# Kernel tuning notes

Measured on AMD Instinct MI355X. Metric: run time of the kernel, lower is better.

Reference implementation:

```python
import jax, jax.numpy as jnp
import numpy as np

H, NOPE, ROPE, VD, KV_LORA, HID = 16, 128, 64, 128, 512, 2048
QK = NOPE + ROPE
SCALE = QK ** -0.5
EPS = 1e-5


def _rope(x, freqs):
    # x: [b, t, h, ROPE]; freqs: [t, ROPE//2] angles. Complex-pair rotation.
    cos = jnp.cos(freqs)[None, :, None, :]
    sin = jnp.sin(freqs)[None, :, None, :]
    xr = x.reshape(x.shape[:-1] + (ROPE // 2, 2))
    x1, x2 = xr[..., 0], xr[..., 1]
    o1 = x1 * cos - x2 * sin
    o2 = x1 * sin + x2 * cos
    return jnp.stack([o1, o2], axis=-1).reshape(x.shape)


def _layernorm(x, g, b):
    mu = jnp.mean(x, axis=-1, keepdims=True)
    var = jnp.var(x, axis=-1, keepdims=True)
    return (x - mu) * jax.lax.rsqrt(var + EPS) * g + b


def setup_inputs() -> dict:
    key = jax.random.key(0)
    ks = jax.random.split(key, 6)
    b, t = 2, 2048

    def xavier(k, shape):
        fan_in, fan_out = shape
        lim = np.sqrt(6.0 / (fan_in + fan_out))
        return jax.random.uniform(k, shape, jnp.float32, -lim, lim)

    hidden_states = jax.random.normal(ks[0], (b, t, HID), jnp.float32)
    # rope angles: theta_i = 10000^(-2i/ROPE), angle[p,i] = p * theta_i
    inv_freq = 1.0 / (10000.0 ** (np.arange(0, ROPE, 2, dtype=np.float32) / ROPE))
    freqs = jnp.asarray(np.arange(t, dtype=np.float32)[:, None] * inv_freq[None, :])
    # causal additive mask broadcastable to [b,t,s,h]
    causal = jnp.where(jnp.arange(t)[None, :] <= jnp.arange(t)[:, None], 0.0, -1e9)
    attention_mask = causal.astype(jnp.float32)[None, :, :, None]
    return {
        "hidden_states": hidden_states,
        "freqs": freqs,
        "attention_mask": attention_mask,
        "Wq": xavier(ks[1], (HID, H * QK)),
        "Wkv_a": xavier(ks[2], (HID, KV_LORA + ROPE)),
        "kv_gamma": jnp.ones((KV_LORA,), jnp.float32),
        "kv_beta": jnp.zeros((KV_LORA,), jnp.float32),
        "Wkv_b": xavier(ks[3], (KV_LORA, H * (NOPE + VD))),
        "Wout": xavier(ks[4], (H * VD, HID)),
    }


def reference(hidden_states, freqs, attention_mask, Wq, Wkv_a, kv_gamma, kv_beta, Wkv_b, Wout):
    b, t, _ = hidden_states.shape
    # Q projection -> [b,t,H,QK], split nope/rope, rotate rope part
    q = (hidden_states @ Wq).reshape(b, t, H, QK)
    q_nope, q_rope = q[..., :NOPE], q[..., NOPE:]
    q_rope = _rope(q_rope, freqs)
    # compressed KV latent + shared rope key
    kv = hidden_states @ Wkv_a                      # [b,t,KV_LORA+ROPE]
    kv_lat, k_rope = kv[..., :KV_LORA], kv[..., KV_LORA:]
    k_rope = _rope(k_rope[:, :, None, :], freqs)    # [b,t,1,ROPE]
    kv_lat = _layernorm(kv_lat, kv_gamma, kv_beta)
    kvb = (kv_lat @ Wkv_b).reshape(b, t, H, NOPE + VD)
    k_nope, v = kvb[..., :NOPE], kvb[..., NOPE:]
    k = jnp.concatenate([k_nope, jnp.broadcast_to(k_rope, (b, t, H, ROPE))], axis=-1)
    q = jnp.concatenate([q_nope, q_rope], axis=-1)
    # scores [b,t,s,h]; NOTE: source applies softmax over dim=-1 == HEAD axis (faithful)
    scores = jnp.einsum("bthd,bshd->btsh", q, k) * SCALE + attention_mask
    weights = jax.nn.softmax(scores.astype(jnp.float32), axis=-1).astype(q.dtype)
    attn = jnp.einsum("btsh,bshd->bthd", weights, v).reshape(b, t, H * VD)
    return attn @ Wout
```

## Files before the change

### kernel.cpp

```cpp
#include <hip/hip_runtime.h>

typedef unsigned short u16;
typedef short bf16x8 __attribute__((ext_vector_type(8)));
typedef float f32x4 __attribute__((ext_vector_type(4)));
typedef float f32x16 __attribute__((ext_vector_type(16)));
typedef unsigned short u16x8 __attribute__((ext_vector_type(8)));

#define GLOBAL_AS __attribute__((address_space(1)))
#define LDS_AS __attribute__((address_space(3)))
#define DEVINL __device__ __forceinline__

#define BATCH 2
#define TSEQ 2048
#define NHEAD 16
#define QK 192
#define VD 128
#define HID 2048
#define MROWS 4096
#define SCALE_QK 0.07216878364870323f

DEVINL float b2f(u16 u) { union { unsigned i; float f; } x; x.i = ((unsigned)u) << 16; return x.f; }
DEVINL u16 f2b(float f) {
    union { float f; unsigned u; } x; x.f = f;
    unsigned r = x.u + 0x7fffu + ((x.u >> 16) & 1u);
    return (u16)(r >> 16);
}
DEVINL void gload_lds16(const u16* g, u16* l) {
    __builtin_amdgcn_global_load_lds((const GLOBAL_AS unsigned*)g, (LDS_AS unsigned*)l, 16, 0, 0);
}
DEVINL unsigned pk2(float a, float b) {
    unsigned d;
    asm("v_cvt_pk_bf16_f32 %0, %1, %2" : "=v"(d) : "v"(a), "v"(b));
    return d;
}


__global__ void cvt_bf16x8(const float* __restrict__ in, u16* __restrict__ out, int n8) {
    int i = blockIdx.x * 256 + threadIdx.x;
    if (i < n8) {
        const float4* p = (const float4*)(in + (size_t)i * 8);
        float4 x = p[0], y = p[1];
        u16x8 o;
        o[0] = f2b(x.x); o[1] = f2b(x.y); o[2] = f2b(x.z); o[3] = f2b(x.w);
        o[4] = f2b(y.x); o[5] = f2b(y.y); o[6] = f2b(y.z); o[7] = f2b(y.w);
        *(u16x8*)(out + (size_t)i * 8) = o;
    }
}

__global__ void rope_tab_k(const float* __restrict__ freqs, float2* __restrict__ tab) {
    int i = blockIdx.x * 256 + threadIdx.x;
    float f = freqs[i], s, c;
    sincosf(f, &s, &c);
    tab[i] = make_float2(c, s);
}

__global__ void transpose_cvt(const float* __restrict__ in, u16* __restrict__ out,
                              int R, int C, int Cpad) {
    __shared__ float tile[32][33];
    int c0 = blockIdx.x * 32, r0 = blockIdx.y * 32;
    int tx = threadIdx.x, ty = threadIdx.y;
#pragma unroll
    for (int j = 0; j < 4; j++) {
        int r = r0 + ty + j * 8, c = c0 + tx;
        tile[ty + j * 8][tx] = (c < C) ? in[(size_t)r * C + c] : 0.f;
    }
    __syncthreads();
#pragma unroll
    for (int j = 0; j < 4; j++) {
        int oc = c0 + ty + j * 8;
        int orr = r0 + tx;
        if (oc < Cpad) out[(size_t)oc * R + orr] = f2b(tile[tx][ty + j * 8]);
    }
}

template<int MODE>
__global__ __launch_bounds__(256)
void gemm_bt(const u16* __restrict__ A, const u16* __restrict__ BT, int Kdim,
             void* __restrict__ out0, void* __restrict__ out1, void* __restrict__ out2,
             const float2* __restrict__ tab) {
    __shared__ __align__(16) u16 As[128 * 32];
    __shared__ __align__(16) u16 Bs[128 * 32];
    const int tid = threadIdx.x, lane = tid & 63, wave = tid >> 6;
    const int m0 = blockIdx.x * 128, n0 = blockIdx.y * 128;
    const int wr = wave >> 1, wc = wave & 1;

    f32x4 acc[4][4];
#pragma unroll
    for (int i = 0; i < 4; i++)
#pragma unroll
        for (int j = 0; j < 4; j++) acc[i][j] = f32x4{0.f, 0.f, 0.f, 0.f};

    const int e0 = (wave * 2 + 0) * 512 + lane * 8;
    const int e1 = (wave * 2 + 1) * 512 + lane * 8;
    const u16* gA0 = A + (size_t)(m0 + (e0 >> 5)) * Kdim + (e0 & 31);
    const u16* gA1 = A + (size_t)(m0 + (e1 >> 5)) * Kdim + (e1 & 31);
    const u16* gB0 = BT + (size_t)(n0 + (e0 >> 5)) * Kdim + (e0 & 31);
    const u16* gB1 = BT + (size_t)(n0 + (e1 >> 5)) * Kdim + (e1 & 31);
    u16* lA0 = &As[(wave * 2 + 0) * 512];
    u16* lA1 = &As[(wave * 2 + 1) * 512];
    u16* lB0 = &Bs[(wave * 2 + 0) * 512];
    u16* lB1 = &Bs[(wave * 2 + 1) * 512];

    const int arow = lane & 15, koff = (lane >> 4) * 8;

    for (int k0 = 0; k0 < Kdim; k0 += 32) {
        gload_lds16(gA0, lA0); gload_lds16(gA1, lA1);
        gload_lds16(gB0, lB0); gload_lds16(gB1, lB1);
        gA0 += 32; gA1 += 32; gB0 += 32; gB1 += 32;
        asm volatile("s_waitcnt vmcnt(0)" ::: "memory");
        __syncthreads();
        bf16x8 af[4], bfr[4];
#pragma unroll
        for (int i = 0; i < 4; i++)
            af[i] = *(const bf16x8*)&As[(wr * 64 + i * 16 + arow) * 32 + koff];
#pragma unroll
        for (int j = 0; j < 4; j++)
            bfr[j] = *(const bf16x8*)&Bs[(wc * 64 + j * 16 + arow) * 32 + koff];
#pragma unroll
        for (int i = 0; i < 4; i++)
#pragma unroll
            for (int j = 0; j < 4; j++)
                acc[i][j] = __builtin_amdgcn_mfma_f32_16x16x32_bf16(af[i], bfr[j], acc[i][j], 0, 0, 0);
        __syncthreads();
    }

#pragma unroll
    for (int i = 0; i < 4; i++)
#pragma unroll
        for (int j = 0; j < 4; j++)
#pragma unroll
            for (int r = 0; r < 4; r++) {
                int row = m0 + wr * 64 + i * 16 + (lane >> 4) * 4 + r;
                int col = n0 + wc * 64 + j * 16 + (lane & 15);
                float v = acc[i][j][r];
                if constexpr (MODE == 0) {
                    int h = col / 192, d = col % 192;
                    int b = row >> 11, t = row & 2047;
                    float vv = v;
                    float pv = __shfl_xor(v, 1);
                    if (d >= 128) {
                        float2 cs = tab[t * 32 + ((d - 128) >> 1)];
                        vv = v * cs.x + pv * ((lane & 1) ? cs.y : -cs.y);
                    }
                    ((u16*)out0)[((size_t)(b * 16 + h) * 2048 + t) * 192 + d] = f2b(vv);
                } else if constexpr (MODE == 1) {
                    ((float*)out0)[(size_t)row * 640 + col] = v;
                } else if constexpr (MODE == 2) {
                    int h = col >> 8, d = col & 255;
                    int b = row >> 11, t = row & 2047;
                    size_t base = (size_t)(b * 16 + h) * 2048 + t;
                    if (d < 128) ((u16*)out0)[base * 192 + d] = f2b(v);
                    else {
                        u16 bv = f2b(v);
                        ((u16*)out1)[base * 128 + (d - 128)] = bv;
                        ((u16*)out2)[((size_t)(b * 16 + h) * 128 + (d - 128)) * 2048 + t] = bv;
                    }
                } else {
                    ((float*)out0)[(size_t)row * 2048 + col] = v;
                }
            }
}

__global__ __launch_bounds__(256)
void ln_krope(const float* __restrict__ kvf, const float* __restrict__ gamma,
              const float* __restrict__ beta, const float2* __restrict__ tab,
              u16* __restrict__ kvlat, u16* __restrict__ kbuf) {
    int row = blockIdx.x, tid = threadIdx.x;
    const float* x = kvf + (size_t)row * 640;
    float v0 = x[tid], v1 = x[tid + 256];
    float s = v0 + v1, sq = v0 * v0 + v1 * v1;
#pragma unroll
    for (int off = 1; off < 64; off <<= 1) { s += __shfl_xor(s, off); sq += __shfl_xor(sq, off); }
    __shared__ float ssum[4], ssq[4];
    if ((tid & 63) == 0) { ssum[tid >> 6] = s; ssq[tid >> 6] = sq; }
    __syncthreads();
    s = ssum[0] + ssum[1] + ssum[2] + ssum[3];
    sq = ssq[0] + ssq[1] + ssq[2] + ssq[3];
    float mu = s * (1.f / 512.f);
    float var = sq * (1.f / 512.f) - mu * mu;
    float rs = rsqrtf(var + 1e-5f);
    kvlat[(size_t)row * 512 + tid] = f2b((v0 - mu) * rs * gamma[tid] + beta[tid]);
    kvlat[(size_t)row * 512 + tid + 256] = f2b((v1 - mu) * rs * gamma[tid + 256] + beta[tid + 256]);
    if (tid < 32) {
        int t = row & 2047, b = row >> 11;
        float x1 = x[512 + 2 * tid], x2 = x[512 + 2 * tid + 1];
        float2 cs = tab[t * 32 + tid];
        u16 u1 = f2b(x1 * cs.x - x2 * cs.y), u2 = f2b(x1 * cs.y + x2 * cs.x);
        for (int h = 0; h < 16; ++h) {
            size_t base = ((size_t)(b * 16 + h) * 2048 + t) * 192 + 128 + 2 * tid;
            kbuf[base] = u1; kbuf[base + 1] = u2;
        }
    }
}

__global__ void suff1(const u16* __restrict__ vbuf, float* __restrict__ psum) {
    int bh = blockIdx.x, c = blockIdx.y, d = threadIdx.x;
    float s = 0.f;
    const u16* vp = vbuf + ((size_t)bh * 2048 + c * 128) * 128 + d;
    for (int tt = 0; tt < 128; ++tt) s += b2f(vp[(size_t)tt * 128]);
    psum[((size_t)bh * 16 + c) * 128 + d] = s;
}
__global__ void suff2(const float* __restrict__ psum, float* __restrict__ csuf) {
    int bh = blockIdx.x, d = threadIdx.x;
    float run = 0.f;
    for (int c = 15; c >= 0; --c) {
        csuf[((size_t)bh * 16 + c) * 128 + d] = run;
        run += psum[((size_t)bh * 16 + c) * 128 + d];
    }
}
__global__ void suff3(const u16* __restrict__ vbuf, const float* __restrict__ csuf,
                      u16* __restrict__ attnb) {
    int bh = blockIdx.x, c = blockIdx.y, d = threadIdx.x;
    int b = bh >> 4, h = bh & 15;
    float run = csuf[((size_t)bh * 16 + c) * 128 + d];
    for (int tt = 127; tt >= 0; --tt) {
        int t = c * 128 + tt;
        attnb[((size_t)b * 2048 + t) * 2048 + h * 128 + d] = f2b(run * 0.0625f);
        run += b2f(vbuf[((size_t)bh * 2048 + t) * 128 + d]);
    }
}

__global__ __launch_bounds__(256, 3)
void z_kernel(const u16* __restrict__ qbuf, const u16* __restrict__ kbuf,
              u16* __restrict__ zbufT) {
    __shared__ __align__(16) u16 Ks[2 * 12288];
    const int tid = threadIdx.x, lane = tid & 63, wave = tid >> 6;
    const int hi = lane >> 5, l31 = lane & 31;
    const int tgrp = wave & 1, sblk = wave >> 1;
    int id = blockIdx.x;
    int b = id & 1, p = id >> 1;
    int tT = 0;
    for (;;) { int cnt = (tT + 2) >> 1; if (p < cnt) break; p -= cnt; ++tT; }
    const int g2 = p * 2;
    const int ns = ((tT + 1 - g2) >= 2) ? 2 : 1;
    const int t0 = tT * 64;
    const int rK = sblk * 32 + l31;
    const int t_loc = tgrp * 32 + l31;

    bf16x8 qA[12];
    auto QLOAD = [&](int h) {
        const u16* qp = qbuf + ((size_t)(b * 16 + h) * 2048 + t0 + t_loc) * 192 + hi * 8;
#pragma unroll
        for (int kk = 0; kk < 12; kk++) qA[kk] = *(const bf16x8*)(qp + kk * 16);
    };
    auto KSTAGE = [&](int h, int st, int bi) {
        const size_t hrow = (size_t)(b * 16 + h) * 2048;
        const int s0 = st * 64;
#pragma unroll
        for (int j2 = 0; j2 < 6; j2++) {
            int idx = (wave * 6 + j2) * 64 + lane;
            int rr2 = idx / 24, cc = idx % 24, cs = cc ^ (rr2 & 7);
            gload_lds16(kbuf + (hrow + s0 + rr2) * 192 + cs * 8, &Ks[bi * 12288 + idx * 8]);
        }
    };
    f32x16 za0, za1;
#pragma unroll
    for (int r = 0; r < 16; r++) { za0[r] = 0.f; za1[r] = 0.f; }
    auto COMPUTE = [&](f32x16& za, const u16* K) {
        f32x16 e;
#pragma unroll
        for (int r = 0; r < 16; r++) e[r] = 0.f;
        __builtin_amdgcn_s_setprio(1);
#pragma unroll
        for (int kk = 0; kk < 12; kk++) {
            int slot = (2 * kk + hi) ^ (rK & 7);
            bf16x8 kf = *(const bf16x8*)&K[rK * 192 + slot * 8];
            e = __builtin_amdgcn_mfma_f32_32x32x16_bf16(kf, qA[kk], e, 0, 0, 0);
        }
        __builtin_amdgcn_s_setprio(0);
#pragma unroll
        for (int r = 0; r < 16; r++) za[r] += __expf(e[r] * SCALE_QK);
    };

    QLOAD(0);
    KSTAGE(0, g2, 0);
    asm volatile("s_waitcnt vmcnt(0)" ::: "memory");
    __builtin_amdgcn_s_barrier();
    int kb = 0;
#pragma unroll 1
    for (int h = 0; h < 16; ++h) {
        if (ns == 2)      KSTAGE(h, g2 + 1, kb ^ 1);
        else if (h < 15)  KSTAGE(h + 1, g2, kb ^ 1);
        if (ns == 2 || h < 15) {
            if (h > 0) { asm volatile("s_waitcnt vmcnt(18)" ::: "memory"); }
            else       { asm volatile("s_waitcnt vmcnt(6)"  ::: "memory"); }
        } else {
            asm volatile("s_waitcnt vmcnt(12)" ::: "memory");
        }
        __builtin_amdgcn_s_barrier();
        __builtin_amdgcn_sched_barrier(0);
        COMPUTE(za0, &Ks[kb * 12288]);
        __builtin_amdgcn_s_barrier();
        if (ns == 1 && h < 15) QLOAD(h + 1);
        kb ^= 1;
        if (ns == 2) {
            if (h < 15) {
                KSTAGE(h + 1, g2, kb ^ 1);
                asm volatile("s_waitcnt vmcnt(6)" ::: "memory");
            } else {
                asm volatile("s_waitcnt vmcnt(0)" ::: "memory");
            }
            __builtin_amdgcn_s_barrier();
            __builtin_amdgcn_sched_barrier(0);
            COMPUTE(za1, &Ks[kb * 12288]);
            __builtin_amdgcn_s_barrier();
            if (h < 15) QLOAD(h + 1);
            kb ^= 1;
        }
    }
#pragma unroll
    for (int r = 0; r < 16; r++) {
        int spat = (r & 3) + 8 * (r >> 2) + 4 * hi;
        int sg = g2 * 64 + sblk * 32 + spat;
        zbufT[((size_t)b * 2048 + sg) * 2048 + t0 + t_loc] = f2b(__fdividef(1.f, za0[r]));
    }
    if (ns == 2) {
#pragma unroll
        for (int r = 0; r < 16; r++) {
            int spat = (r & 3) + 8 * (r >> 2) + 4 * hi;
            int sg = (g2 + 1) * 64 + sblk * 32 + spat;
            zbufT[((size_t)b * 2048 + sg) * 2048 + t0 + t_loc] = f2b(__fdividef(1.f, za1[r]));
        }
    }
}

__global__ __launch_bounds__(512, 1)
void attn_pv(const u16* __restrict__ qbuf, const u16* __restrict__ kbuf,
             const u16* __restrict__ vtbuf, const u16* __restrict__ zbufT,
             u16* __restrict__ attnb) {
    __shared__ __align__(16) u16 lds[57344];
    u16* Ks = lds;
    u16* Vt = lds + 24576;
    u16* Zs = lds + 40960;
    const int tid = threadIdx.x, lane = tid & 63, wave = tid >> 6;
    const int hi = lane >> 5, l31 = lane & 31;
    const int tgrp = wave & 3, sblk = wave >> 2;
    int id = blockIdx.x;
    int xcd = id & 7, j2 = id >> 3;
    int pr = j2 & 7, g = j2 >> 3;
    int bh = xcd * 4 + g;
    const int b = bh >> 4, h = bh & 15;
    const size_t kvrow = (size_t)bh * 2048;
    const int rK = sblk * 32 + l31;
    const int t_loc = tgrp * 32 + l31;
    const int zg = t_loc >> 3, zoff = t_loc & 7;

    for (int part = 0; part < 2; ++part) {
        const int T = part ? (15 - pr) : pr;
        const int t0p = T * 128, nst = 2 * T + 2;
        const int tg = t0p + t_loc;

        bf16x8 qf[12];
        {
            const u16* qp = qbuf + (kvrow + tg) * 192 + hi * 8;
#pragma unroll
            for (int kk = 0; kk < 12; kk++) qf[kk] = *(const bf16x8*)(qp + kk * 16);
        }
        f32x16 o[4];
#pragma unroll
        for (int db = 0; db < 4; db++)
#pragma unroll
            for (int r = 0; r < 16; r++) o[db][r] = 0.f;

        auto STAGE = [&](int st, int bi) {
            const int s0 = st * 64;
#pragma unroll
            for (int j = 0; j < 3; j++) {
                int idx = (wave * 3 + j) * 64 + lane;
                int rr2 = idx / 24, cc = idx % 24, cs = cc ^ (rr2 & 7);
                gload_lds16(kbuf + (kvrow + s0 + rr2) * 192 + cs * 8, &Ks[bi * 12288 + idx * 8]);
            }
#pragma unroll
            for (int j = 0; j < 2; j++) {
                int idx = (wave * 2 + j) * 64 + lane;
                int d = idx >> 3, cc = idx & 7, cs = cc ^ (d & 7);
                gload_lds16(vtbuf + ((size_t)bh * 128 + d) * 2048 + s0 + cs * 8, &Vt[bi * 8192 + idx * 8]);
            }
#pragma unroll
            for (int j = 0; j < 2; j++) {
                int idx = (wave * 2 + j) * 64 + lane;
                int sr = idx >> 4, cc = idx & 15, cs = cc ^ (sr & 15);
                gload_lds16(zbufT + ((size_t)b * 2048 + s0 + sr) * 2048 + t0p + cs * 8, &Zs[bi * 8192 + idx * 8]);
            }
        };
        STAGE(0, 0);
        for (int st = 0; st < nst; ++st) {
            int cur = st & 1;
            if (st + 1 < nst) {
                STAGE(st + 1, cur ^ 1);
                asm volatile("s_waitcnt vmcnt(7)" ::: "memory");
            } else {
                asm volatile("s_waitcnt vmcnt(0)" ::: "memory");
            }
            __builtin_amdgcn_s_barrier();
            __builtin_amdgcn_sched_barrier(0);
            const u16* Kc = &Ks[cur * 12288];
            const u16* Vc = &Vt[cur * 8192];
            const u16* Zc = &Zs[cur * 8192];
            f32x16 sacc;
#pragma unroll
            for (int r = 0; r < 16; r++) sacc[r] = 0.f;
            __builtin_amdgcn_s_setprio(1);
#pragma unroll
            for (int kk = 0; kk < 12; kk++) {
                int slot = (2 * kk + hi) ^ (rK & 7);
                bf16x8 kf = *(const bf16x8*)&Kc[rK * 192 + slot * 8];
                sacc = __builtin_amdgcn_mfma_f32_32x32x16_bf16(kf, qf[kk], sacc, 0, 0, 0);
            }
            __builtin_amdgcn_s_setprio(0);
            const int s0g = st * 64 + sblk * 32;
            float w[16];
#pragma unroll
            for (int r = 0; r < 16; r++) {
                int spat = (r & 3) + 8 * (r >> 2) + 4 * hi;
                int sr = sblk * 32 + spat;
                float rz = b2f(Zc[sr * 128 + ((zg ^ (sr & 15)) << 3) + zoff]);
                w[r] = (s0g + spat <= tg) ? __expf(sacc[r] * SCALE_QK) * rz : 0.f;
            }
            unsigned pw0 = pk2(w[0], w[1]), pw1 = pk2(w[2], w[3]);
            unsigned pw2 = pk2(w[4], w[5]), pw3 = pk2(w[6], w[7]);
            unsigned pw4 = pk2(w[8], w[9]), pw5 = pk2(w[10], w[11]);
            unsigned pw6 = pk2(w[12], w[13]), pw7 = pk2(w[14], w[15]);
            unsigned a0 = pw0, a1 = pw1, a2 = pw4, a3 = pw5;
            asm volatile("v_permlane32_swap_b32 %0, %1" : "+v"(a0), "+v"(pw2));
            asm volatile("v_permlane32_swap_b32 %0, %1" : "+v"(a1), "+v"(pw3));
            asm volatile("v_permlane32_swap_b32 %0, %1" : "+v"(a2), "+v"(pw6));
            asm volatile("v_permlane32_swap_b32 %0, %1" : "+v"(a3), "+v"(pw7));
            union PU { unsigned u[4]; bf16x8 v; } p0, p1;
            p0.u[0] = a0;  p0.u[1] = a1;  p0.u[2] = pw2; p0.u[3] = pw3;
            p1.u[0] = a2;  p1.u[1] = a3;  p1.u[2] = pw6; p1.u[3] = pw7;
            __builtin_amdgcn_s_setprio(1);
#pragma unroll
            for (int db = 0; db < 4; db++) {
                int dv = db * 32 + l31;
#pragma unroll
                for (int ks = 0; ks < 2; ks++) {
                    int slot = (sblk * 4 + 2 * ks + hi) ^ (dv & 7);
                    bf16x8 vb = *(const bf16x8*)&Vc[dv * 64 + slot * 8];
                    o[db] = __builtin_amdgcn_mfma_f32_32x32x16_bf16(ks ? p1.v : p0.v, vb, o[db], 0, 0, 0);
                }
            }
            __builtin_amdgcn_s_setprio(0);
            __builtin_amdgcn_s_barrier();
        }
        __syncthreads();
        float* red = (float*)lds;
        if (sblk == 0) {
#pragma unroll
            for (int db = 0; db < 4; db++)
#pragma unroll
                for (int r = 0; r < 16; r++) {
                    int trow = (r & 3) + 8 * (r >> 2) + 4 * hi;
                    red[(tgrp * 32 + trow) * 128 + db * 32 + l31] = o[db][r];
                }
        }
        __syncthreads();
        if (sblk == 1) {
#pragma unroll
            for (int db = 0; db < 4; db++)
#pragma unroll
                for (int r = 0; r < 16; r++) {
                    int trow = (r & 3) + 8 * (r >> 2) + 4 * hi;
                    float val = o[db][r] + red[(tgrp * 32 + trow) * 128 + db * 32 + l31];
                    size_t oi = ((size_t)b * 2048 + t0p + tgrp * 32 + trow) * 2048 + h * 128 + db * 32 + l31;
                    attnb[oi] = f2b(val + b2f(attnb[oi]));
                }
        }
        __syncthreads();
    }
}

extern "C" void kernel_launch(void* const* d_in, const int* in_sizes, int n_in,
                              void* d_out, int out_size, void* d_ws, size_t ws_size,
                              hipStream_t stream) {
    (void)in_sizes; (void)n_in; (void)out_size;
    const float* hidden = (const float*)d_in[0];
    const float* freqs  = (const float*)d_in[1];
    const float* Wq     = (const float*)d_in[3];
    const float* Wkva   = (const float*)d_in[4];
    const float* gamma  = (const float*)d_in[5];
    const float* beta   = (const float*)d_in[6];
    const float* Wkvb   = (const float*)d_in[7];
    const float* Wout   = (const float*)d_in[8];
    float* outp = (float*)d_out;

    char* ws = (char*)d_ws;
    size_t off = 0;
    auto alloc = [&](size_t bytes) -> void* {
        void* p = ws + off; off += (bytes + 255) & ~(size_t)255; return p;
    };
    u16*   hid_b = (u16*)alloc((size_t)MROWS * HID * 2);
    u16*   WqT   = (u16*)alloc((size_t)3072 * 2048 * 2);
    u16*   WkvaT = (u16*)alloc((size_t)640 * 2048 * 2);
    u16*   WkvbT = (u16*)alloc((size_t)4096 * 512 * 2);
    u16*   WoutT = (u16*)alloc((size_t)2048 * 2048 * 2);
    u16*   qbuf  = (u16*)alloc((size_t)BATCH * NHEAD * TSEQ * QK * 2);
    float* kvf   = (float*)alloc((size_t)MROWS * 640 * 4);
    u16*   kvlat = (u16*)alloc((size_t)MROWS * 512 * 2);
    u16*   kbuf  = (u16*)alloc((size_t)BATCH * NHEAD * TSEQ * QK * 2);
    u16*   vbuf  = (u16*)alloc((size_t)BATCH * NHEAD * TSEQ * VD * 2);
    u16*   attnb = (u16*)alloc((size_t)MROWS * 2048 * 2);
    float2* ropetab = (float2*)alloc((size_t)2048 * 32 * 8);
    float* psum  = (float*)alloc((size_t)32 * 16 * 128 * 4);
    float* csuf  = (float*)alloc((size_t)32 * 16 * 128 * 4);
    if (off > ws_size) return;
    u16* zbufT = WqT;
    u16* vtbuf = hid_b;

    cvt_bf16x8<<<4096, 256, 0, stream>>>(hidden, hid_b, MROWS * HID / 8);
    rope_tab_k<<<256, 256, 0, stream>>>(freqs, ropetab);
    dim3 tb(32, 8);
    transpose_cvt<<<dim3(96, 64), tb, 0, stream>>>(Wq, WqT, 2048, 3072, 3072);
    transpose_cvt<<<dim3(20, 64), tb, 0, stream>>>(Wkva, WkvaT, 2048, 576, 640);
    transpose_cvt<<<dim3(128, 16), tb, 0, stream>>>(Wkvb, WkvbT, 512, 4096, 4096);
    transpose_cvt<<<dim3(64, 64), tb, 0, stream>>>(Wout, WoutT, 2048, 2048, 2048);

    gemm_bt<1><<<dim3(32, 5), 256, 0, stream>>>(hid_b, WkvaT, 2048, kvf, nullptr, nullptr, nullptr);
    gemm_bt<0><<<dim3(32, 24), 256, 0, stream>>>(hid_b, WqT, 2048, qbuf, nullptr, nullptr, ropetab);
    ln_krope<<<MROWS, 256, 0, stream>>>(kvf, gamma, beta, ropetab, kvlat, kbuf);
    gemm_bt<2><<<dim3(32, 32), 256, 0, stream>>>(kvlat, WkvbT, 512, kbuf, vbuf, vtbuf, nullptr);

    suff1<<<dim3(32, 16), 128, 0, stream>>>(vbuf, psum);
    suff2<<<32, 128, 0, stream>>>(psum, csuf);
    suff3<<<dim3(32, 16), 128, 0, stream>>>(vbuf, csuf, attnb);

    z_kernel<<<544, 256, 0, stream>>>(qbuf, kbuf, zbufT);
    attn_pv<<<256, 512, 0, stream>>>(qbuf, kbuf, vtbuf, zbufT, attnb);

    gemm_bt<3><<<dim3(32, 16), 256, 0, stream>>>(attnb, WoutT, 2048, outp, nullptr, nullptr, nullptr);
}
```

Baseline: 514.1 us.

## Store softmax normalizer row-major by query and load it directly into registers

The z_kernel now writes the reciprocal head-softmax normalizers in a [b, t, s] layout using 8-byte vector stores, replacing scattered 2-byte stores into the transposed buffer. attn_pv no longer stages Z tiles through LDS. Each lane prefetches its four u16x4 Z chunks for the next tile into registers, and the wait count is adjusted to match. This cuts LDS footprint and the LDS reads on the softmax path, in exchange for uncoalesced-ish global reads with a 4KB stride per lane and extra register pressure.

```diff
diff --git a/kernel.cpp b/kernel.cpp
--- a/kernel.cpp
+++ b/kernel.cpp
@@ -5,6 +5,7 @@
 typedef float f32x4 __attribute__((ext_vector_type(4)));
 typedef float f32x16 __attribute__((ext_vector_type(16)));
 typedef unsigned short u16x8 __attribute__((ext_vector_type(8)));
+typedef unsigned short u16x4 __attribute__((ext_vector_type(4)));
 
 #define GLOBAL_AS __attribute__((address_space(1)))
 #define LDS_AS __attribute__((address_space(3)))
@@ -222,7 +223,7 @@
 
 __global__ __launch_bounds__(256, 3)
 void z_kernel(const u16* __restrict__ qbuf, const u16* __restrict__ kbuf,
-              u16* __restrict__ zbufT) {
+              u16* __restrict__ ztb) {
     __shared__ __align__(16) u16 Ks[2 * 12288];
     const int tid = threadIdx.x, lane = tid & 63, wave = tid >> 6;
     const int hi = lane >> 5, l31 = lane & 31;
@@ -308,30 +309,32 @@
             kb ^= 1;
         }
     }
-#pragma unroll
-    for (int r = 0; r < 16; r++) {
-        int spat = (r & 3) + 8 * (r >> 2) + 4 * hi;
-        int sg = g2 * 64 + sblk * 32 + spat;
-        zbufT[((size_t)b * 2048 + sg) * 2048 + t0 + t_loc] = f2b(__fdividef(1.f, za0[r]));
+    const size_t trow = ((size_t)b * 2048 + t0 + t_loc) * 2048;
+#pragma unroll
+    for (int g3 = 0; g3 < 4; g3++) {
+        u16x4 zo;
+#pragma unroll
+        for (int j = 0; j < 4; j++) zo[j] = f2b(__fdividef(1.f, za0[g3 * 4 + j]));
+        *(u16x4*)&ztb[trow + g2 * 64 + sblk * 32 + 4 * hi + 8 * g3] = zo;
     }
     if (ns == 2) {
 #pragma unroll
-        for (int r = 0; r < 16; r++) {
-            int spat = (r & 3) + 8 * (r >> 2) + 4 * hi;
-            int sg = (g2 + 1) * 64 + sblk * 32 + spat;
-            zbufT[((size_t)b * 2048 + sg) * 2048 + t0 + t_loc] = f2b(__fdividef(1.f, za1[r]));
+        for (int g3 = 0; g3 < 4; g3++) {
+            u16x4 zo;
+#pragma unroll
+            for (int j = 0; j < 4; j++) zo[j] = f2b(__fdividef(1.f, za1[g3 * 4 + j]));
+            *(u16x4*)&ztb[trow + (g2 + 1) * 64 + sblk * 32 + 4 * hi + 8 * g3] = zo;
         }
     }
 }
 
 __global__ __launch_bounds__(512, 1)
 void attn_pv(const u16* __restrict__ qbuf, const u16* __restrict__ kbuf,
-             const u16* __restrict__ vtbuf, const u16* __restrict__ zbufT,
+             const u16* __restrict__ vtbuf, const u16* __restrict__ ztb,
              u16* __restrict__ attnb) {
-    __shared__ __align__(16) u16 lds[57344];
+    __shared__ __align__(16) u16 lds[40960];
     u16* Ks = lds;
     u16* Vt = lds + 24576;
-    u16* Zs = lds + 40960;
     const int tid = threadIdx.x, lane = tid & 63, wave = tid >> 6;
     const int hi = lane >> 5, l31 = lane & 31;
     const int tgrp = wave & 3, sblk = wave >> 2;
@@ -343,12 +346,13 @@
     const size_t kvrow = (size_t)bh * 2048;
     const int rK = sblk * 32 + l31;
     const int t_loc = tgrp * 32 + l31;
-    const int zg = t_loc >> 3, zoff = t_loc & 7;
 
     for (int part = 0; part < 2; ++part) {
         const int T = part ? (15 - pr) : pr;
         const int t0p = T * 128, nst = 2 * T + 2;
         const int tg = t0p + t_loc;
+        const u16* zrow = ztb + ((size_t)b * 2048 + tg) * 2048;
+        const int zbase0 = sblk * 32 + 4 * hi;
 
         bf16x8 qf[12];
         {
@@ -376,19 +380,23 @@
                 int d = idx >> 3, cc = idx & 7, cs = cc ^ (d & 7);
                 gload_lds16(vtbuf + ((size_t)bh * 128 + d) * 2048 + s0 + cs * 8, &Vt[bi * 8192 + idx * 8]);
             }
-#pragma unroll
-            for (int j = 0; j < 2; j++) {
-                int idx = (wave * 2 + j) * 64 + lane;
-                int sr = idx >> 4, cc = idx & 15, cs = cc ^ (sr & 15);
-                gload_lds16(zbufT + ((size_t)b * 2048 + s0 + sr) * 2048 + t0p + cs * 8, &Zs[bi * 8192 + idx * 8]);
-            }
+        };
+        u16x4 zc0, zc1, zc2, zc3, zn0, zn1, zn2, zn3;
+        auto ZLOAD = [&](int st, u16x4& a, u16x4& bb, u16x4& c, u16x4& d) {
+            int base = st * 64 + zbase0;
+            a  = *(const u16x4*)(zrow + base);
+            bb = *(const u16x4*)(zrow + base + 8);
+            c  = *(const u16x4*)(zrow + base + 16);
+            d  = *(const u16x4*)(zrow + base + 24);
         };
         STAGE(0, 0);
+        ZLOAD(0, zc0, zc1, zc2, zc3);
         for (int st = 0; st < nst; ++st) {
             int cur = st & 1;
             if (st + 1 < nst) {
                 STAGE(st + 1, cur ^ 1);
-                asm volatile("s_waitcnt vmcnt(7)" ::: "memory");
+                ZLOAD(st + 1, zn0, zn1, zn2, zn3);
+                asm volatile("s_waitcnt vmcnt(9)" ::: "memory");
             } else {
                 asm volatile("s_waitcnt vmcnt(0)" ::: "memory");
             }
@@ -396,7 +404,6 @@
             __builtin_amdgcn_sched_barrier(0);
             const u16* Kc = &Ks[cur * 12288];
             const u16* Vc = &Vt[cur * 8192];
-            const u16* Zc = &Zs[cur * 8192];
             f32x16 sacc;
 #pragma unroll
             for (int r = 0; r < 16; r++) sacc[r] = 0.f;
@@ -410,13 +417,16 @@
             __builtin_amdgcn_s_setprio(0);
             const int s0g = st * 64 + sblk * 32;
             float w[16];
-#pragma unroll
-            for (int r = 0; r < 16; r++) {
-                int spat = (r & 3) + 8 * (r >> 2) + 4 * hi;
-                int sr = sblk * 32 + spat;
-                float rz = b2f(Zc[sr * 128 + ((zg ^ (sr & 15)) << 3) + zoff]);
-                w[r] = (s0g + spat <= tg) ? __expf(sacc[r] * SCALE_QK) * rz : 0.f;
-            }
+#define SMG(g3, zcv)                                                        \
+_Pragma("unroll")                                                           \
+            for (int j = 0; j < 4; j++) {                                   \
+                int r = g3 * 4 + j;                                         \
+                int spat = j + 8 * g3 + 4 * hi;                             \
+                w[r] = (s0g + spat <= tg)                                   \
+                     ? __expf(sacc[r] * SCALE_QK) * b2f(zcv[j]) : 0.f;      \
+            }
+            SMG(0, zc0) SMG(1, zc1) SMG(2, zc2) SMG(3, zc3)
+#undef SMG
             unsigned pw0 = pk2(w[0], w[1]), pw1 = pk2(w[2], w[3]);
             unsigned pw2 = pk2(w[4], w[5]), pw3 = pk2(w[6], w[7]);
             unsigned pw4 = pk2(w[8], w[9]), pw5 = pk2(w[10], w[11]);
@@ -442,6 +452,7 @@
             }
             __builtin_amdgcn_s_setprio(0);
             __builtin_amdgcn_s_barrier();
+            if (st + 1 < nst) { zc0 = zn0; zc1 = zn1; zc2 = zn2; zc3 = zn3; }
         }
         __syncthreads();
         float* red = (float*)lds;
@@ -504,7 +515,7 @@
     float* psum  = (float*)alloc((size_t)32 * 16 * 128 * 4);
     float* csuf  = (float*)alloc((size_t)32 * 16 * 128 * 4);
     if (off > ws_size) return;
-    u16* zbufT = WqT;
+    u16* ztb   = WqT;
     u16* vtbuf = hid_b;
 
     cvt_bf16x8<<<4096, 256, 0, stream>>>(hidden, hid_b, MROWS * HID / 8);
@@ -524,8 +535,8 @@
     suff2<<<32, 128, 0, stream>>>(psum, csuf);
     suff3<<<dim3(32, 16), 128, 0, stream>>>(vbuf, csuf, attnb);
 
-    z_kernel<<<544, 256, 0, stream>>>(qbuf, kbuf, zbufT);
-    attn_pv<<<256, 512, 0, stream>>>(qbuf, kbuf, vtbuf, zbufT, attnb);
+    z_kernel<<<544, 256, 0, stream>>>(qbuf, kbuf, ztb);
+    attn_pv<<<256, 512, 0, stream>>>(qbuf, kbuf, vtbuf, ztb, attnb);
 
     gemm_bt<3><<<dim3(32, 16), 256, 0, stream>>>(attnb, WoutT, 2048, outp, nullptr, nullptr, nullptr);
 }
```

Result: faster. 493.0 us (-4.1%).
